# Kernel optimization log

Hardware: AMD Instinct MI355X
Metric: run time of the kernel (lower is better)

## Reference

```python
import jax, jax.numpy as jnp
import numpy as np

N_NODES = 100000
N_EDGES = 1600000
D_IN = 64
D_HID = 64
D_OUT = 64
DROP_P = 0.5


def _degree_norms(src, dst, n):
    ones = jnp.ones(src.shape[0], dtype=jnp.float32)
    deg_out = jax.ops.segment_sum(ones, src, num_segments=n)  # out-degree of src nodes
    deg_in = jax.ops.segment_sum(ones, dst, num_segments=n)   # in-degree of dst nodes
    norm_src = jnp.where(deg_out > 0, jax.lax.rsqrt(jnp.maximum(deg_out, 1.0)), 0.0)
    norm_dst = jnp.where(deg_in > 0, jax.lax.rsqrt(jnp.maximum(deg_in, 1.0)), 0.0)
    return norm_src, norm_dst


def _graph_conv(h, W, b, src, dst, norm_src, norm_dst, n, activation=None):
    # DGL GraphConv, norm='both': out = D_in^{-1/2} A (D_out^{-1/2} h) W + b
    h = h * norm_src[:, None]
    h = h @ W                      # small GEMM first (in >= out), math-equivalent
    msg = h[src]                   # gather  [E, d]
    agg = jax.ops.segment_sum(msg, dst, num_segments=n)  # scatter-add [N, d]
    out = agg * norm_dst[:, None] + b
    if activation is not None:
        out = activation(out)
    return out


def _dropout(h, key, p=DROP_P):
    keep = jax.random.bernoulli(key, 1.0 - p, h.shape)
    return jnp.where(keep, h / (1.0 - p), 0.0)


def setup_inputs() -> dict:
    key = jax.random.key(0)
    ks = jax.random.split(key, 6)
    x = jax.random.normal(ks[0], (N_NODES, D_IN), dtype=jnp.float32)
    W0 = jax.random.normal(ks[1], (D_IN, D_HID), dtype=jnp.float32) * 0.05
    W1 = jax.random.normal(ks[2], (D_HID, D_HID), dtype=jnp.float32) * 0.05
    W2 = jax.random.normal(ks[3], (D_HID, D_OUT), dtype=jnp.float32) * 0.05
    b0 = jnp.zeros((D_HID,), dtype=jnp.float32)
    b1 = jnp.zeros((D_HID,), dtype=jnp.float32)
    b2 = jnp.zeros((D_OUT,), dtype=jnp.float32)
    src = jax.random.randint(ks[4], (N_EDGES,), 0, N_NODES, dtype=jnp.int32)
    dst = jax.random.randint(ks[5], (N_EDGES,), 0, N_NODES, dtype=jnp.int32)
    return {"x": x, "W0": W0, "b0": b0, "W1": W1, "b1": b1, "W2": W2, "b2": b2,
            "src": src, "dst": dst}


def reference(x, W0, b0, W1, b1, W2, b2, src, dst):
    n = x.shape[0]
    norm_src, norm_dst = _degree_norms(src, dst, n)
    dk = jax.random.key(1)
    h = _graph_conv(x, W0, b0, src, dst, norm_src, norm_dst, n, jax.nn.relu)
    h = _dropout(h, jax.random.fold_in(dk, 0))
    h = _graph_conv(h, W1, b1, src, dst, norm_src, norm_dst, n, jax.nn.relu)
    h = _dropout(h, jax.random.fold_in(dk, 1))
    h = _graph_conv(h, W2, b2, src, dst, norm_src, norm_dst, n, None)
    return h
```

## Files before the change

kernel.cpp:

```cpp
#include <hip/hip_runtime.h>
#include <hip/hip_bf16.h>
#include <hip/hip_fp16.h>
#include <cstddef>


#define WG 256
#define SLOT_S 48
#define NB_SHIFT 9
#define NB_W 512
#define EB 2048
#define PSTRIDE 257

__host__ __device__ static inline unsigned rotl32(unsigned x, int r) {
  return (x << r) | (x >> (32 - r));
}

__host__ __device__ static inline void threefry2x32(unsigned k0, unsigned k1,
                                                    unsigned x0, unsigned x1,
                                                    unsigned& o0, unsigned& o1) {
  unsigned ks2 = k0 ^ k1 ^ 0x1BD11BDAu;
  x0 += k0; x1 += k1;
#define TF_ROUND(r) { x0 += x1; x1 = rotl32(x1, r); x1 ^= x0; }
  TF_ROUND(13) TF_ROUND(15) TF_ROUND(26) TF_ROUND(6)
  x0 += k1;  x1 += ks2 + 1u;
  TF_ROUND(17) TF_ROUND(29) TF_ROUND(16) TF_ROUND(24)
  x0 += ks2; x1 += k0 + 2u;
  TF_ROUND(13) TF_ROUND(15) TF_ROUND(26) TF_ROUND(6)
  x0 += k0;  x1 += k1 + 3u;
  TF_ROUND(17) TF_ROUND(29) TF_ROUND(16) TF_ROUND(24)
  x0 += k1;  x1 += ks2 + 4u;
  TF_ROUND(13) TF_ROUND(15) TF_ROUND(26) TF_ROUND(6)
  x0 += ks2; x1 += k0 + 5u;
#undef TF_ROUND
  o0 = x0; o1 = x1;
}

__device__ static inline float2 h2f(unsigned u) {
  return __half22float2(__builtin_bit_cast(__half2, u));
}
__device__ static inline unsigned f2h(float a, float b) {
  return __builtin_bit_cast(unsigned, __floats2half2_rn(a, b));
}


__global__ __launch_bounds__(WG) void bin_k(
    const int* __restrict__ src, const int* __restrict__ dst,
    unsigned* __restrict__ binbuf_d, unsigned short* __restrict__ binbuf_s,
    unsigned short* __restrict__ pref_d, unsigned short* __restrict__ pref_s,
    int e) {
  __shared__ int hist_d[256], hist_s[256];
  __shared__ int scan_d[256], scan_s[256];
  __shared__ int curs_d[256], curs_s[256];
  __shared__ unsigned sorted_d[EB];
  __shared__ unsigned short sorted_s[EB];
  int tid = threadIdx.x;
  int blk = blockIdx.x;
  int base = blk * EB;
  int cnt = e - base;
  if (cnt > EB) cnt = EB;

  hist_d[tid] = 0;
  hist_s[tid] = 0;
  __syncthreads();
  for (int i = tid; i < cnt; i += WG) {
    int d = dst[base + i];
    int s = src[base + i];
    atomicAdd(&hist_d[d >> NB_SHIFT], 1);
    atomicAdd(&hist_s[s >> NB_SHIFT], 1);
  }
  __syncthreads();
  int hd = hist_d[tid], hs = hist_s[tid];
  scan_d[tid] = hd;
  scan_s[tid] = hs;
  __syncthreads();
  for (int st = 1; st < 256; st <<= 1) {
    int ad = (tid >= st) ? scan_d[tid - st] : 0;
    int as = (tid >= st) ? scan_s[tid - st] : 0;
    __syncthreads();
    scan_d[tid] += ad;
    scan_s[tid] += as;
    __syncthreads();
  }
  int ed = scan_d[tid] - hd;
  int es = scan_s[tid] - hs;
  curs_d[tid] = ed;
  curs_s[tid] = es;
  pref_d[(size_t)blk * PSTRIDE + tid] = (unsigned short)ed;
  pref_s[(size_t)blk * PSTRIDE + tid] = (unsigned short)es;
  if (tid == 255) {
    pref_d[(size_t)blk * PSTRIDE + 256] = (unsigned short)scan_d[255];
    pref_s[(size_t)blk * PSTRIDE + 256] = (unsigned short)scan_s[255];
  }
  __syncthreads();
  for (int i = tid; i < cnt; i += WG) {
    int d = dst[base + i];
    int s = src[base + i];
    int pd = atomicAdd(&curs_d[d >> NB_SHIFT], 1);
    sorted_d[pd] = ((unsigned)(d & (NB_W - 1)) << 17) | (unsigned)s;
    int ps = atomicAdd(&curs_s[s >> NB_SHIFT], 1);
    sorted_s[ps] = (unsigned short)(s & (NB_W - 1));
  }
  __syncthreads();
  for (int i = tid; i < cnt; i += WG) binbuf_d[base + i] = sorted_d[i];
  for (int i = tid; i < cnt; i += WG) binbuf_s[base + i] = sorted_s[i];
}


__global__ __launch_bounds__(WG) void debin_k(
    const unsigned* __restrict__ binbuf_d,
    const unsigned short* __restrict__ binbuf_s,
    const unsigned short* __restrict__ pref_d,
    const unsigned short* __restrict__ pref_s,
    int* __restrict__ slot, int* __restrict__ cnt_in,
    float* __restrict__ nsrc, const float* __restrict__ x,
    unsigned short* __restrict__ G0, int n, int nblk, int nbuck) {
  __shared__ int lcnt[NB_W];
  __shared__ float lns[NB_W];
  int tid = threadIdx.x;
  int b = blockIdx.x;
  for (int i = tid; i < NB_W; i += WG) lcnt[i] = 0;
  __syncthreads();
  if (b < nbuck) {
    for (int seg = tid; seg < nblk; seg += WG) {
      const unsigned short* pr = pref_d + (size_t)seg * PSTRIDE + b;
      int p0 = pr[0], p1 = pr[1];
      const unsigned* bb = binbuf_d + (size_t)seg * EB;
      for (int i = p0; i < p1; ++i) {
        unsigned v = bb[i];
        int dl = v >> 17;
        int s = (int)(v & 0x1FFFFu);
        int c = atomicAdd(&lcnt[dl], 1);
        if (c < SLOT_S) slot[(size_t)((b << NB_SHIFT) + dl) * SLOT_S + c] = s;
      }
    }
    __syncthreads();
    for (int i = tid; i < NB_W; i += WG) {
      int v = (b << NB_SHIFT) + i;
      if (v < n) cnt_in[v] = lcnt[i];
    }
  } else {
    int b2 = b - nbuck;
    for (int seg = tid; seg < nblk; seg += WG) {
      const unsigned short* pr = pref_s + (size_t)seg * PSTRIDE + b2;
      int p0 = pr[0], p1 = pr[1];
      const unsigned short* bb = binbuf_s + (size_t)seg * EB;
      for (int i = p0; i < p1; ++i) atomicAdd(&lcnt[bb[i]], 1);
    }
    __syncthreads();
    int vbase = b2 << NB_SHIFT;
    for (int i = tid; i < NB_W; i += WG) {
      int v = vbase + i;
      if (v < n) {
        int c = lcnt[i];
        float ns = (c > 0) ? rsqrtf((float)c) : 0.f;
        lns[i] = ns;
        nsrc[v] = ns;
      }
    }
    __syncthreads();
    const float4* x4 = (const float4*)x;
    uint2* G2 = (uint2*)G0;
    int lim = NB_W * 16;
    for (int idx = tid; idx < lim; idx += WG) {
      int nl = idx >> 4;
      int v = vbase + nl;
      if (v < n) {
        float ns = lns[nl];
        float4 r = x4[(size_t)v * 16 + (idx & 15)];
        G2[(size_t)v * 16 + (idx & 15)] =
            make_uint2(f2h(r.x * ns, r.y * ns), f2h(r.z * ns, r.w * ns));
      }
    }
  }
}

__global__ __launch_bounds__(WG) void layer_k(
    const unsigned short* __restrict__ G, const int* __restrict__ slot,
    const int* __restrict__ cnt_in, const float* __restrict__ nsrc,
    const float* __restrict__ W, const float* __restrict__ bias,
    unsigned short* __restrict__ GoutH, float* __restrict__ GoutF,
    int n, int mid, unsigned dk0, unsigned dk1) {
  __shared__ float4 Ws[1024];
  __shared__ __align__(16) float rows[4][272];
  const float4* W4 = (const float4*)W;
  for (int i = threadIdx.x; i < 1024; i += WG) Ws[i] = W4[i];

  int wave = threadIdx.x >> 6;
  int lane = threadIdx.x & 63;
  int g = lane >> 4;
  int l16 = lane & 15;
  int v = blockIdx.x * 16 + wave * 4 + g;
  bool valid = (v < n);
  int vc = valid ? v : (n - 1);

  int degt = valid ? cnt_in[vc] : 0;
  int deg = (degt > SLOT_S) ? SLOT_S : degt;
  const int* sl = slot + (size_t)vc * SLOT_S;
  const uint2* G2 = (const uint2*)G;

  float4 aA = make_float4(0.f, 0.f, 0.f, 0.f);
  float4 aB = make_float4(0.f, 0.f, 0.f, 0.f);
  float4 aC = make_float4(0.f, 0.f, 0.f, 0.f);
  float4 aD = make_float4(0.f, 0.f, 0.f, 0.f);
#define ACC(dst, m) { float2 lo = h2f((m).x), hi = h2f((m).y); \
    dst.x += lo.x; dst.y += lo.y; dst.z += hi.x; dst.w += hi.y; }
  int nq = deg >> 2;
  int i = 0;
  for (; i + 1 < nq; i += 2) {
    int4 q0 = *(const int4*)(sl + i * 4);
    int4 q1 = *(const int4*)(sl + i * 4 + 4);
    uint2 m0 = G2[(size_t)q0.x * 16 + l16];
    uint2 m1 = G2[(size_t)q0.y * 16 + l16];
    uint2 m2 = G2[(size_t)q0.z * 16 + l16];
    uint2 m3 = G2[(size_t)q0.w * 16 + l16];
    uint2 m4 = G2[(size_t)q1.x * 16 + l16];
    uint2 m5 = G2[(size_t)q1.y * 16 + l16];
    uint2 m6 = G2[(size_t)q1.z * 16 + l16];
    uint2 m7 = G2[(size_t)q1.w * 16 + l16];
    ACC(aA, m0) ACC(aB, m1) ACC(aC, m2) ACC(aD, m3)
    ACC(aA, m4) ACC(aB, m5) ACC(aC, m6) ACC(aD, m7)
  }
  if (i < nq) {
    int4 q0 = *(const int4*)(sl + i * 4);
    uint2 m0 = G2[(size_t)q0.x * 16 + l16];
    uint2 m1 = G2[(size_t)q0.y * 16 + l16];
    uint2 m2 = G2[(size_t)q0.z * 16 + l16];
    uint2 m3 = G2[(size_t)q0.w * 16 + l16];
    ACC(aA, m0) ACC(aB, m1) ACC(aC, m2) ACC(aD, m3)
  }
  int rem = deg & 3;
  if (rem) {
    int4 q = *(const int4*)(sl + (deg & ~3));
    int s0 = q.x;
    int s1 = (rem > 1) ? q.y : s0;
    int s2 = (rem > 2) ? q.z : s0;
    float w1 = (rem > 1) ? 1.f : 0.f;
    float w2 = (rem > 2) ? 1.f : 0.f;
    uint2 m0 = G2[(size_t)s0 * 16 + l16];
    uint2 m1 = G2[(size_t)s1 * 16 + l16];
    uint2 m2 = G2[(size_t)s2 * 16 + l16];
    ACC(aA, m0)
    { float2 lo = h2f(m1.x), hi = h2f(m1.y);
      aB.x = fmaf(w1, lo.x, aB.x); aB.y = fmaf(w1, lo.y, aB.y);
      aB.z = fmaf(w1, hi.x, aB.z); aB.w = fmaf(w1, hi.y, aB.w); }
    { float2 lo = h2f(m2.x), hi = h2f(m2.y);
      aC.x = fmaf(w2, lo.x, aC.x); aC.y = fmaf(w2, lo.y, aC.y);
      aC.z = fmaf(w2, hi.x, aC.z); aC.w = fmaf(w2, hi.y, aC.w); }
  }
#undef ACC
  float4 agg;
  agg.x = (aA.x + aB.x) + (aC.x + aD.x);
  agg.y = (aA.y + aB.y) + (aC.y + aD.y);
  agg.z = (aA.z + aB.z) + (aC.z + aD.z);
  agg.w = (aA.w + aB.w) + (aC.w + aD.w);

  float* rw = &rows[wave][g * 68];
  *(float4*)(rw + l16 * 4) = agg;
  __syncthreads();

  float4 acc = make_float4(0.f, 0.f, 0.f, 0.f);
#pragma unroll
  for (int k = 0; k < 64; ++k) {
    float a = rw[k];
    float4 w = Ws[k * 16 + l16];
    acc.x = fmaf(a, w.x, acc.x);
    acc.y = fmaf(a, w.y, acc.y);
    acc.z = fmaf(a, w.z, acc.z);
    acc.w = fmaf(a, w.w, acc.w);
  }

  float nd = (degt > 0) ? rsqrtf((float)degt) : 0.f;
  float4 b4 = ((const float4*)bias)[l16];
  float4 o;
  o.x = fmaf(acc.x, nd, b4.x);
  o.y = fmaf(acc.y, nd, b4.y);
  o.z = fmaf(acc.z, nd, b4.z);
  o.w = fmaf(acc.w, nd, b4.w);
  if (mid) {
    o.x = fmaxf(o.x, 0.f); o.y = fmaxf(o.y, 0.f);
    o.z = fmaxf(o.z, 0.f); o.w = fmaxf(o.w, 0.f);
    unsigned idx = (unsigned)(v * 64 + l16 * 4);
    unsigned r0a, r0b, r1a, r1b, r2a, r2b, r3a, r3b;
    threefry2x32(dk0, dk1, 0u, idx + 0u, r0a, r0b);
    threefry2x32(dk0, dk1, 0u, idx + 1u, r1a, r1b);
    threefry2x32(dk0, dk1, 0u, idx + 2u, r2a, r2b);
    threefry2x32(dk0, dk1, 0u, idx + 3u, r3a, r3b);
    float ns2 = 2.f * nsrc[vc];
    o.x = ((r0a ^ r0b) & 0x80000000u) ? 0.f : o.x * ns2;
    o.y = ((r1a ^ r1b) & 0x80000000u) ? 0.f : o.y * ns2;
    o.z = ((r2a ^ r2b) & 0x80000000u) ? 0.f : o.z * ns2;
    o.w = ((r3a ^ r3b) & 0x80000000u) ? 0.f : o.w * ns2;
    if (valid)
      ((uint2*)GoutH)[(size_t)v * 16 + l16] =
          make_uint2(f2h(o.x, o.y), f2h(o.z, o.w));
  } else {
    if (valid) ((float4*)GoutF)[(size_t)v * 16 + l16] = o;
  }
}


extern "C" void kernel_launch(void* const* d_in, const int* in_sizes, int n_in,
                              void* d_out, int out_size, void* d_ws, size_t ws_size,
                              hipStream_t stream) {
  const float* x  = (const float*)d_in[0];
  const float* W0 = (const float*)d_in[1];
  const float* b0 = (const float*)d_in[2];
  const float* W1 = (const float*)d_in[3];
  const float* b1 = (const float*)d_in[4];
  const float* W2 = (const float*)d_in[5];
  const float* b2 = (const float*)d_in[6];
  const int* src  = (const int*)d_in[7];
  const int* dst  = (const int*)d_in[8];
  float* out = (float*)d_out;

  const int n = in_sizes[0] / 64;
  const int e = in_sizes[7];
  const int nbuck = (n + NB_W - 1) / NB_W;
  const int nblk = (e + EB - 1) / EB;

  char* w = (char*)d_ws;
  size_t off = 0;
  auto alloc = [&](size_t bytes) -> void* {
    void* p = w + off;
    off += (bytes + 255) & ~(size_t)255;
    return p;
  };
  int*            cnt_in   = (int*)alloc((size_t)n * 4);
  float*          nsrc     = (float*)alloc((size_t)n * 4);
  unsigned*       binbuf_d = (unsigned*)alloc((size_t)nblk * EB * 4);
  unsigned short* binbuf_s = (unsigned short*)alloc((size_t)nblk * EB * 2);
  unsigned short* pref_d   = (unsigned short*)alloc((size_t)nblk * PSTRIDE * 2);
  unsigned short* pref_s   = (unsigned short*)alloc((size_t)nblk * PSTRIDE * 2);
  int*            slot     = (int*)alloc((size_t)nbuck * NB_W * SLOT_S * 4);
  unsigned short* G0       = (unsigned short*)alloc((size_t)n * 64 * 2);
  unsigned short* G1       = (unsigned short*)alloc((size_t)n * 64 * 2);

  unsigned k0a, k0b, k1a, k1b;
  threefry2x32(0u, 1u, 0u, 0u, k0a, k0b);
  threefry2x32(0u, 1u, 0u, 1u, k1a, k1b);

  const int gL = (n + 15) / 16;

  bin_k<<<nblk, WG, 0, stream>>>(src, dst, binbuf_d, binbuf_s,
                                 pref_d, pref_s, e);
  debin_k<<<2 * nbuck, WG, 0, stream>>>(binbuf_d, binbuf_s, pref_d, pref_s,
                                        slot, cnt_in, nsrc, x, G0,
                                        n, nblk, nbuck);

  layer_k<<<gL, WG, 0, stream>>>(G0, slot, cnt_in, nsrc, W0, b0, G1, nullptr,
                                 n, 1, k0a, k0b);
  layer_k<<<gL, WG, 0, stream>>>(G1, slot, cnt_in, nsrc, W1, b1, G0, nullptr,
                                 n, 1, k1a, k1b);
  layer_k<<<gL, WG, 0, stream>>>(G0, slot, cnt_in, nsrc, W2, b2, nullptr, out,
                                 n, 0, 0u, 0u);
}
```

Baseline: 293.4 us.

## Replace two-pass edge binning with direct global atomics for CSR slot build

Result: slower. 396.8 us (+35.2%).

```diff
diff --git a/kernel.cpp b/kernel.cpp
--- a/kernel.cpp
+++ b/kernel.cpp
@@ -6,10 +6,6 @@
 
 #define WG 256
 #define SLOT_S 48
-#define NB_SHIFT 9
-#define NB_W 512
-#define EB 2048
-#define PSTRIDE 257
 
 __host__ __device__ static inline unsigned rotl32(unsigned x, int r) {
   return (x << r) | (x >> (32 - r));
@@ -43,135 +39,50 @@
 }
 
 
-__global__ __launch_bounds__(WG) void bin_k(
+__global__ __launch_bounds__(WG) void edge_k(
     const int* __restrict__ src, const int* __restrict__ dst,
-    unsigned* __restrict__ binbuf_d, unsigned short* __restrict__ binbuf_s,
-    unsigned short* __restrict__ pref_d, unsigned short* __restrict__ pref_s,
-    int e) {
-  __shared__ int hist_d[256], hist_s[256];
-  __shared__ int scan_d[256], scan_s[256];
-  __shared__ int curs_d[256], curs_s[256];
-  __shared__ unsigned sorted_d[EB];
-  __shared__ unsigned short sorted_s[EB];
-  int tid = threadIdx.x;
-  int blk = blockIdx.x;
-  int base = blk * EB;
-  int cnt = e - base;
-  if (cnt > EB) cnt = EB;
-
-  hist_d[tid] = 0;
-  hist_s[tid] = 0;
-  __syncthreads();
-  for (int i = tid; i < cnt; i += WG) {
-    int d = dst[base + i];
-    int s = src[base + i];
-    atomicAdd(&hist_d[d >> NB_SHIFT], 1);
-    atomicAdd(&hist_s[s >> NB_SHIFT], 1);
-  }
-  __syncthreads();
-  int hd = hist_d[tid], hs = hist_s[tid];
-  scan_d[tid] = hd;
-  scan_s[tid] = hs;
-  __syncthreads();
-  for (int st = 1; st < 256; st <<= 1) {
-    int ad = (tid >= st) ? scan_d[tid - st] : 0;
-    int as = (tid >= st) ? scan_s[tid - st] : 0;
-    __syncthreads();
-    scan_d[tid] += ad;
-    scan_s[tid] += as;
-    __syncthreads();
-  }
-  int ed = scan_d[tid] - hd;
-  int es = scan_s[tid] - hs;
-  curs_d[tid] = ed;
-  curs_s[tid] = es;
-  pref_d[(size_t)blk * PSTRIDE + tid] = (unsigned short)ed;
-  pref_s[(size_t)blk * PSTRIDE + tid] = (unsigned short)es;
-  if (tid == 255) {
-    pref_d[(size_t)blk * PSTRIDE + 256] = (unsigned short)scan_d[255];
-    pref_s[(size_t)blk * PSTRIDE + 256] = (unsigned short)scan_s[255];
-  }
-  __syncthreads();
-  for (int i = tid; i < cnt; i += WG) {
-    int d = dst[base + i];
-    int s = src[base + i];
-    int pd = atomicAdd(&curs_d[d >> NB_SHIFT], 1);
-    sorted_d[pd] = ((unsigned)(d & (NB_W - 1)) << 17) | (unsigned)s;
-    int ps = atomicAdd(&curs_s[s >> NB_SHIFT], 1);
-    sorted_s[ps] = (unsigned short)(s & (NB_W - 1));
-  }
-  __syncthreads();
-  for (int i = tid; i < cnt; i += WG) binbuf_d[base + i] = sorted_d[i];
-  for (int i = tid; i < cnt; i += WG) binbuf_s[base + i] = sorted_s[i];
-}
-
-
-__global__ __launch_bounds__(WG) void debin_k(
-    const unsigned* __restrict__ binbuf_d,
-    const unsigned short* __restrict__ binbuf_s,
-    const unsigned short* __restrict__ pref_d,
-    const unsigned short* __restrict__ pref_s,
-    int* __restrict__ slot, int* __restrict__ cnt_in,
-    float* __restrict__ nsrc, const float* __restrict__ x,
-    unsigned short* __restrict__ G0, int n, int nblk, int nbuck) {
-  __shared__ int lcnt[NB_W];
-  __shared__ float lns[NB_W];
-  int tid = threadIdx.x;
-  int b = blockIdx.x;
-  for (int i = tid; i < NB_W; i += WG) lcnt[i] = 0;
-  __syncthreads();
-  if (b < nbuck) {
-    for (int seg = tid; seg < nblk; seg += WG) {
-      const unsigned short* pr = pref_d + (size_t)seg * PSTRIDE + b;
-      int p0 = pr[0], p1 = pr[1];
-      const unsigned* bb = binbuf_d + (size_t)seg * EB;
-      for (int i = p0; i < p1; ++i) {
-        unsigned v = bb[i];
-        int dl = v >> 17;
-        int s = (int)(v & 0x1FFFFu);
-        int c = atomicAdd(&lcnt[dl], 1);
-        if (c < SLOT_S) slot[(size_t)((b << NB_SHIFT) + dl) * SLOT_S + c] = s;
-      }
+    int* __restrict__ deg_out, int* __restrict__ cnt_in,
+    int* __restrict__ slot, int e) {
+  int i0 = (blockIdx.x * WG + threadIdx.x) * 4;
+  if (i0 + 3 < e) {
+    int4 s4 = *(const int4*)(src + i0);
+    int4 d4 = *(const int4*)(dst + i0);
+    atomicAdd(&deg_out[s4.x], 1);
+    atomicAdd(&deg_out[s4.y], 1);
+    atomicAdd(&deg_out[s4.z], 1);
+    atomicAdd(&deg_out[s4.w], 1);
+    int c0 = atomicAdd(&cnt_in[d4.x], 1);
+    int c1 = atomicAdd(&cnt_in[d4.y], 1);
+    int c2 = atomicAdd(&cnt_in[d4.z], 1);
+    int c3 = atomicAdd(&cnt_in[d4.w], 1);
+    if (c0 < SLOT_S) slot[(size_t)d4.x * SLOT_S + c0] = s4.x;
+    if (c1 < SLOT_S) slot[(size_t)d4.y * SLOT_S + c1] = s4.y;
+    if (c2 < SLOT_S) slot[(size_t)d4.z * SLOT_S + c2] = s4.z;
+    if (c3 < SLOT_S) slot[(size_t)d4.w * SLOT_S + c3] = s4.w;
+  } else {
+    for (int i = i0; i < e; ++i) {
+      int s = src[i];
+      int d = dst[i];
+      atomicAdd(&deg_out[s], 1);
+      int c = atomicAdd(&cnt_in[d], 1);
+      if (c < SLOT_S) slot[(size_t)d * SLOT_S + c] = s;
     }
-    __syncthreads();
-    for (int i = tid; i < NB_W; i += WG) {
-      int v = (b << NB_SHIFT) + i;
-      if (v < n) cnt_in[v] = lcnt[i];
-    }
-  } else {
-    int b2 = b - nbuck;
-    for (int seg = tid; seg < nblk; seg += WG) {
-      const unsigned short* pr = pref_s + (size_t)seg * PSTRIDE + b2;
-      int p0 = pr[0], p1 = pr[1];
-      const unsigned short* bb = binbuf_s + (size_t)seg * EB;
-      for (int i = p0; i < p1; ++i) atomicAdd(&lcnt[bb[i]], 1);
-    }
-    __syncthreads();
-    int vbase = b2 << NB_SHIFT;
-    for (int i = tid; i < NB_W; i += WG) {
-      int v = vbase + i;
-      if (v < n) {
-        int c = lcnt[i];
-        float ns = (c > 0) ? rsqrtf((float)c) : 0.f;
-        lns[i] = ns;
-        nsrc[v] = ns;
-      }
-    }
-    __syncthreads();
-    const float4* x4 = (const float4*)x;
-    uint2* G2 = (uint2*)G0;
-    int lim = NB_W * 16;
-    for (int idx = tid; idx < lim; idx += WG) {
-      int nl = idx >> 4;
-      int v = vbase + nl;
-      if (v < n) {
-        float ns = lns[nl];
-        float4 r = x4[(size_t)v * 16 + (idx & 15)];
-        G2[(size_t)v * 16 + (idx & 15)] =
-            make_uint2(f2h(r.x * ns, r.y * ns), f2h(r.z * ns, r.w * ns));
-      }
-    }
-  }
+  }
+}
+
+
+__global__ __launch_bounds__(WG) void ns_k(
+    const int* __restrict__ deg_out, const float* __restrict__ x,
+    float* __restrict__ nsrc, unsigned short* __restrict__ G0, int n) {
+  int idx = blockIdx.x * WG + threadIdx.x;
+  int v = idx >> 4;
+  if (v >= n) return;
+  int c = deg_out[v];
+  float ns = (c > 0) ? rsqrtf((float)c) : 0.f;
+  if ((idx & 15) == 0) nsrc[v] = ns;
+  float4 r = ((const float4*)x)[(size_t)v * 16 + (idx & 15)];
+  ((uint2*)G0)[(size_t)v * 16 + (idx & 15)] =
+      make_uint2(f2h(r.x * ns, r.y * ns), f2h(r.z * ns, r.w * ns));
 }
 
 __global__ __launch_bounds__(WG) void layer_k(
@@ -315,8 +226,6 @@
 
   const int n = in_sizes[0] / 64;
   const int e = in_sizes[7];
-  const int nbuck = (n + NB_W - 1) / NB_W;
-  const int nblk = (e + EB - 1) / EB;
 
   char* w = (char*)d_ws;
   size_t off = 0;
@@ -325,13 +234,11 @@
     off += (bytes + 255) & ~(size_t)255;
     return p;
   };
-  int*            cnt_in   = (int*)alloc((size_t)n * 4);
+  int*            counters = (int*)alloc((size_t)2 * n * 4);
+  int*            cnt_in   = counters;
+  int*            deg_out  = counters + n;
   float*          nsrc     = (float*)alloc((size_t)n * 4);
-  unsigned*       binbuf_d = (unsigned*)alloc((size_t)nblk * EB * 4);
-  unsigned short* binbuf_s = (unsigned short*)alloc((size_t)nblk * EB * 2);
-  unsigned short* pref_d   = (unsigned short*)alloc((size_t)nblk * PSTRIDE * 2);
-  unsigned short* pref_s   = (unsigned short*)alloc((size_t)nblk * PSTRIDE * 2);
-  int*            slot     = (int*)alloc((size_t)nbuck * NB_W * SLOT_S * 4);
+  int*            slot     = (int*)alloc((size_t)n * SLOT_S * 4);
   unsigned short* G0       = (unsigned short*)alloc((size_t)n * 64 * 2);
   unsigned short* G1       = (unsigned short*)alloc((size_t)n * 64 * 2);
 
@@ -339,13 +246,13 @@
   threefry2x32(0u, 1u, 0u, 0u, k0a, k0b);
   threefry2x32(0u, 1u, 0u, 1u, k1a, k1b);
 
+  const int gE = (e / 4 + WG - 1) / WG;
+  const int gN = (n * 16 + WG - 1) / WG;
   const int gL = (n + 15) / 16;
 
-  bin_k<<<nblk, WG, 0, stream>>>(src, dst, binbuf_d, binbuf_s,
-                                 pref_d, pref_s, e);
-  debin_k<<<2 * nbuck, WG, 0, stream>>>(binbuf_d, binbuf_s, pref_d, pref_s,
-                                        slot, cnt_in, nsrc, x, G0,
-                                        n, nblk, nbuck);
+  hipMemsetAsync(counters, 0, (size_t)2 * n * 4, stream);
+  edge_k<<<gE, WG, 0, stream>>>(src, dst, deg_out, cnt_in, slot, e);
+  ns_k<<<gN, WG, 0, stream>>>(deg_out, x, nsrc, G0, n);
 
   layer_k<<<gL, WG, 0, stream>>>(G0, slot, cnt_in, nsrc, W0, b0, G1, nullptr,
                                  n, 1, k0a, k0b);
```
